# Kernel optimization log

Measured on AMD Instinct MI355X. Metric: run time of the kernel, lower is better.

Reference implementation:

```python
import jax, jax.numpy as jnp
import numpy as np

HEADS = 16
DIM_HEAD = 64
EPS = 1e-5


def _layernorm(x, w, b):
    mu = jnp.mean(x, axis=-1, keepdims=True)
    var = jnp.var(x, axis=-1, keepdims=True)
    return (x - mu) * jax.lax.rsqrt(var + EPS) * w + b


def setup_inputs() -> dict:
    key = jax.random.key(0)
    ks = jax.random.split(key, 6)
    B, F, Q, D = 8, 4096, 64, 1024
    inner = HEADS * DIM_HEAD  # 1024
    s = 0.02
    return {
        "features": jax.random.normal(ks[0], (B, F, D), jnp.float32),
        "latents": jax.random.normal(ks[1], (B, Q, D), jnp.float32),
        "lnm_w": jnp.ones((D,), jnp.float32),
        "lnm_b": jnp.zeros((D,), jnp.float32),
        "lnl_w": jnp.ones((D,), jnp.float32),
        "lnl_b": jnp.zeros((D,), jnp.float32),
        "Wq": jax.random.normal(ks[2], (D, inner), jnp.float32) * s,
        "Wk": jax.random.normal(ks[3], (D, inner), jnp.float32) * s,
        "Wv": jax.random.normal(ks[4], (D, inner), jnp.float32) * s,
        "Wo": jax.random.normal(ks[5], (inner, D), jnp.float32) * s,
    }


def reference(features, latents, lnm_w, lnm_b, lnl_w, lnl_b, Wq, Wk, Wv, Wo):
    B, Q = latents.shape[0], latents.shape[1]
    scale = DIM_HEAD ** (-0.5)

    x = _layernorm(features, lnm_w, lnm_b)           # (B, F, D)
    lat = _layernorm(latents, lnl_w, lnl_b)          # (B, Q, D)

    q = (lat @ Wq).reshape(B, Q, HEADS, DIM_HEAD).transpose(0, 2, 1, 3)  # b h q d
    kv_in = jnp.concatenate([x, lat], axis=1)        # (B, F+Q, D)
    FL = kv_in.shape[1]
    k = (kv_in @ Wk).reshape(B, FL, HEADS, DIM_HEAD).transpose(0, 2, 1, 3)  # b h f d
    v = (kv_in @ Wv).reshape(B, FL, HEADS, DIM_HEAD).transpose(0, 2, 1, 3)  # b h f d

    sim = jnp.einsum('bhqd,bhfd->bhqf', q * scale, k)
    alphas = jax.nn.softmax(sim, axis=-1)            # amax-subtract is folded into stable softmax
    out = jnp.einsum('bhqf,bhfv->bhqv', alphas, v)
    out = out.transpose(0, 2, 1, 3).reshape(B, Q, HEADS * DIM_HEAD)
    return out @ Wo
```

## Files before the change

### kernel.cpp

```cpp
#include <hip/hip_runtime.h>


typedef float   f32x4  __attribute__((ext_vector_type(4)));
typedef short   bf16x8 __attribute__((ext_vector_type(8)));

#define MFMA_BF16 __builtin_amdgcn_mfma_f32_16x16x32_bf16

__device__ __forceinline__ unsigned short f2bf(float f) {
  unsigned u = __float_as_uint(f);
  unsigned r = (u + 0x7fffu + ((u >> 16) & 1u)) >> 16;
  return (unsigned short)r;
}

__device__ __forceinline__ void gload_lds16(const unsigned short* g, unsigned short* l) {
  __builtin_amdgcn_global_load_lds(
      (const __attribute__((address_space(1))) unsigned int*)g,
      (__attribute__((address_space(3))) unsigned int*)l, 16, 0, 0);
}

__global__ __launch_bounds__(256) void ln_kernel(
    const float* __restrict__ features, const float* __restrict__ latents,
    const float* __restrict__ lnm_w, const float* __restrict__ lnm_b,
    const float* __restrict__ lnl_w, const float* __restrict__ lnl_b,
    unsigned short* __restrict__ kv_ln, unsigned short* __restrict__ lat_ln)
{
  const int row = blockIdx.x;
  const int b  = row / 4160;
  const int fi = row - b * 4160;
  const bool is_lat = fi >= 4096;
  const float* x = is_lat ? (latents + (size_t)(b * 64 + fi - 4096) * 1024)
                          : (features + (size_t)(b * 4096 + fi) * 1024);
  const float* wp = is_lat ? lnl_w : lnm_w;
  const float* bp = is_lat ? lnl_b : lnm_b;
  const int tid = threadIdx.x;

  float4 v = *(const float4*)(x + tid * 4);
  float s  = v.x + v.y + v.z + v.w;
  float s2 = v.x * v.x + v.y * v.y + v.z * v.z + v.w * v.w;
#pragma unroll
  for (int sh = 1; sh < 64; sh <<= 1) {
    s  += __shfl_xor(s,  sh, 64);
    s2 += __shfl_xor(s2, sh, 64);
  }
  __shared__ float red[8];
  if ((tid & 63) == 0) { red[tid >> 6] = s; red[4 + (tid >> 6)] = s2; }
  __syncthreads();
  s  = red[0] + red[1] + red[2] + red[3];
  s2 = red[4] + red[5] + red[6] + red[7];
  const float mu   = s * (1.0f / 1024.0f);
  const float var  = s2 * (1.0f / 1024.0f) - mu * mu;
  const float rstd = rsqrtf(var + 1e-5f);

  float4 w4 = *(const float4*)(wp + tid * 4);
  float4 b4 = *(const float4*)(bp + tid * 4);
  ushort4 o;
  o.x = f2bf((v.x - mu) * rstd * w4.x + b4.x);
  o.y = f2bf((v.y - mu) * rstd * w4.y + b4.y);
  o.z = f2bf((v.z - mu) * rstd * w4.z + b4.z);
  o.w = f2bf((v.w - mu) * rstd * w4.w + b4.w);
  *(ushort4*)(kv_ln + (size_t)row * 1024 + tid * 4) = o;
  if (is_lat)
    *(ushort4*)(lat_ln + (size_t)(b * 64 + fi - 4096) * 1024 + tid * 4) = o;
}

__global__ __launch_bounds__(256) void wcast_kernel(
    const float* __restrict__ Wq, const float* __restrict__ Wk,
    const float* __restrict__ Wv, const float* __restrict__ Wo,
    unsigned short* __restrict__ Wkv_t, unsigned short* __restrict__ Wq_t,
    unsigned short* __restrict__ Wo_t)
{
  __shared__ float tile[32][33];
  const int kt = blockIdx.x * 32, nt = blockIdx.y * 32;
  const int tx = threadIdx.x & 31, ty = threadIdx.x >> 5;

  const float* src; int nc; float scale = 1.0f;
  if (nt < 1024)      { src = Wk; nc = nt; }
  else if (nt < 2048) { src = Wv; nc = nt - 1024; }
  else if (nt < 3072) { src = Wq; nc = nt - 2048; scale = 0.125f; }
  else                { src = Wo; nc = nt - 3072; }

#pragma unroll
  for (int kk = 0; kk < 4; ++kk)
    tile[ty + kk * 8][tx] = src[(size_t)(kt + ty + kk * 8) * 1024 + nc + tx] * scale;
  __syncthreads();

#pragma unroll
  for (int nn = 0; nn < 4; ++nn) {
    const int ng = nt + ty + nn * 8;
    unsigned short* d;
    if (ng < 2048)      d = Wkv_t + (size_t)ng * 1024;
    else if (ng < 3072) d = Wq_t + (size_t)(ng - 2048) * 1024;
    else                d = Wo_t + (size_t)(ng - 3072) * 1024;
    d[kt + tx] = f2bf(tile[tx][ty + nn * 8]);
  }
}

__global__ __launch_bounds__(1024, 4) void gemm256_bf16(
    const unsigned short* __restrict__ A,
    const unsigned short* __restrict__ Bt,
    unsigned short* __restrict__ Kp, unsigned short* __restrict__ Vp,
    int M, int N, int K)
{
  __shared__ __align__(16) unsigned short lds[65536];
  const int tid  = threadIdx.x;
  const int wave = tid >> 6, lane = tid & 63;
  const int lo = lane & 15, hi = lane >> 4;
  const int wr = wave >> 2, wc = wave & 3;

  const int nbn = gridDim.x;
  int flat = blockIdx.y * nbn + blockIdx.x;
  const int nwg = nbn * gridDim.y;
  flat = (flat & 7) * (nwg >> 3) + (flat >> 3);
  const int bm = flat / nbn, bn = flat - bm * nbn;

  int srow, scol;
  {
    int off = tid * 16;
    int p = off ^ (((off >> 9) & 1) << 5);
    srow = ((p >> 10) << 4) + ((p & 1023) >> 6);
    scol = (p & 63) >> 1;
  }
  const unsigned short* pA = A  + (size_t)(bm * 256 + srow) * K + scol;
  const unsigned short* pB = Bt + (size_t)(bn * 256 + srow) * K + scol;

  f32x4 acc[4][4];
#pragma unroll
  for (int i = 0; i < 4; ++i)
#pragma unroll
    for (int j = 0; j < 4; ++j) acc[i][j] = (f32x4){0.f, 0.f, 0.f, 0.f};

  const int NT = K >> 5;

  gload_lds16(pA,      lds + 0 * 16384 + wave * 512);
  gload_lds16(pB,      lds + 0 * 16384 + 8192 + wave * 512);
  gload_lds16(pA + 32, lds + 1 * 16384 + wave * 512);
  gload_lds16(pB + 32, lds + 1 * 16384 + 8192 + wave * 512);
  asm volatile("s_waitcnt vmcnt(2)" ::: "memory");
  asm volatile("s_barrier" ::: "memory");

  const int swz = (lo * 32 + hi * 8) ^ ((lo & 8) << 1);

#define GPHASE(T, BUF, SBUF)                                                   \
  do {                                                                         \
    const bool st = (T) + 2 < NT;                                              \
    const unsigned short* bp = lds + (BUF) * 16384;                            \
    bf16x8 b0 = *(const bf16x8*)(bp + 8192 + (wc * 4 + 0) * 512 + swz);        \
    bf16x8 b1 = *(const bf16x8*)(bp + 8192 + (wc * 4 + 1) * 512 + swz);        \
    bf16x8 b2 = *(const bf16x8*)(bp + 8192 + (wc * 4 + 2) * 512 + swz);        \
    bf16x8 b3 = *(const bf16x8*)(bp + 8192 + (wc * 4 + 3) * 512 + swz);        \
    bf16x8 a0 = *(const bf16x8*)(bp + (wr * 4 + 0) * 512 + swz);               \
    bf16x8 a1 = *(const bf16x8*)(bp + (wr * 4 + 1) * 512 + swz);               \
    bf16x8 a2 = *(const bf16x8*)(bp + (wr * 4 + 2) * 512 + swz);               \
    bf16x8 a3 = *(const bf16x8*)(bp + (wr * 4 + 3) * 512 + swz);               \
    if (st) gload_lds16(pA + ((T) + 2) * 32, lds + (SBUF) * 16384 + wave * 512); \
    __builtin_amdgcn_s_setprio(1);                                             \
    acc[0][0] = MFMA_BF16(a0, b0, acc[0][0], 0, 0, 0);                         \
    acc[0][1] = MFMA_BF16(a0, b1, acc[0][1], 0, 0, 0);                         \
    acc[0][2] = MFMA_BF16(a0, b2, acc[0][2], 0, 0, 0);                         \
    acc[0][3] = MFMA_BF16(a0, b3, acc[0][3], 0, 0, 0);                         \
    acc[1][0] = MFMA_BF16(a1, b0, acc[1][0], 0, 0, 0);                         \
    acc[1][1] = MFMA_BF16(a1, b1, acc[1][1], 0, 0, 0);                         \
    acc[1][2] = MFMA_BF16(a1, b2, acc[1][2], 0, 0, 0);                         \
    acc[1][3] = MFMA_BF16(a1, b3, acc[1][3], 0, 0, 0);                         \
    __builtin_amdgcn_s_setprio(0);                                             \
    if (st) gload_lds16(pB + ((T) + 2) * 32, lds + (SBUF) * 16384 + 8192 + wave * 512); \
    __builtin_amdgcn_s_setprio(1);                                             \
    acc[2][0] = MFMA_BF16(a2, b0, acc[2][0], 0, 0, 0);                         \
    acc[2][1] = MFMA_BF16(a2, b1, acc[2][1], 0, 0, 0);                         \
    acc[2][2] = MFMA_BF16(a2, b2, acc[2][2], 0, 0, 0);                         \
    acc[2][3] = MFMA_BF16(a2, b3, acc[2][3], 0, 0, 0);                         \
    acc[3][0] = MFMA_BF16(a3, b0, acc[3][0], 0, 0, 0);                         \
    acc[3][1] = MFMA_BF16(a3, b1, acc[3][1], 0, 0, 0);                         \
    acc[3][2] = MFMA_BF16(a3, b2, acc[3][2], 0, 0, 0);                         \
    acc[3][3] = MFMA_BF16(a3, b3, acc[3][3], 0, 0, 0);                         \
    __builtin_amdgcn_s_setprio(0);                                             \
    if (st)                 { asm volatile("s_waitcnt vmcnt(2)" ::: "memory"); } \
    else if ((T) + 1 < NT)  { asm volatile("s_waitcnt vmcnt(0)" ::: "memory"); } \
    asm volatile("s_barrier" ::: "memory");                                    \
  } while (0)

  for (int t = 0; t < NT; t += 4) {
    GPHASE(t + 0, 0, 2);
    GPHASE(t + 1, 1, 3);
    GPHASE(t + 2, 2, 0);
    GPHASE(t + 3, 3, 1);
  }
#undef GPHASE

#pragma unroll
  for (int m = 0; m < 4; ++m) {
    const int grow0 = bm * 256 + wr * 64 + m * 16 + hi * 4;
#pragma unroll
    for (int n = 0; n < 4; ++n) {
      const int cfull = bn * 256 + wc * 64 + n * 16 + lo;
      unsigned short* plane = (cfull & 1024) ? Vp : Kp;
      const size_t pbase = (size_t)((cfull >> 6) & 15) * 2129920 + (cfull & 63);
#pragma unroll
      for (int r = 0; r < 4; ++r)
        plane[pbase + (size_t)(grow0 + r) * 64] = f2bf(acc[m][n][r]);
    }
  }
}

template <typename CT>
__global__ __launch_bounds__(256) void gemm_tn(
    const unsigned short* __restrict__ A,
    const unsigned short* __restrict__ Bt,
    CT* __restrict__ C, int M, int N, int K)
{
  __shared__ __align__(16) unsigned short sA[2][128 * 32];
  __shared__ __align__(16) unsigned short sB[2][128 * 32];
  const int tid  = threadIdx.x;
  const int wave = tid >> 6, lane = tid & 63;
  const int bm = blockIdx.y, bn = blockIdx.x;
  const int wr = wave >> 1, wc = wave & 1;
  const int lo = lane & 15, hi = lane >> 4;
  const int srow = lane >> 2, squad = lane & 3;

  const unsigned short* gA = A  + (size_t)(bm * 128 + srow) * K + squad * 8;
  const unsigned short* gB = Bt + (size_t)(bn * 128 + srow) * K + squad * 8;

  f32x4 acc[4][4];
#pragma unroll
  for (int i = 0; i < 4; ++i)
#pragma unroll
    for (int j = 0; j < 4; ++j) acc[i][j] = (f32x4){0.f, 0.f, 0.f, 0.f};

  const int kt = K >> 5;
#pragma unroll
  for (int c = 0; c < 2; ++c) {
    const int chunk = wave * 2 + c;
    gload_lds16(gA + (size_t)chunk * 16 * K, &sA[0][chunk * 512]);
    gload_lds16(gB + (size_t)chunk * 16 * K, &sB[0][chunk * 512]);
  }
  __syncthreads();

  int buf = 0;
  for (int t = 0; t < kt; ++t) {
    if (t + 1 < kt) {
      const int k0 = (t + 1) << 5;
#pragma unroll
      for (int c = 0; c < 2; ++c) {
        const int chunk = wave * 2 + c;
        gload_lds16(gA + (size_t)chunk * 16 * K + k0, &sA[buf ^ 1][chunk * 512]);
        gload_lds16(gB + (size_t)chunk * 16 * K + k0, &sB[buf ^ 1][chunk * 512]);
      }
    }
    bf16x8 af[4], bfr[4];
#pragma unroll
    for (int i = 0; i < 4; ++i) {
      af[i]  = *(const bf16x8*)&sA[buf][(wr * 64 + i * 16 + lo) * 32 + hi * 8];
      bfr[i] = *(const bf16x8*)&sB[buf][(wc * 64 + i * 16 + lo) * 32 + hi * 8];
    }
#pragma unroll
    for (int i = 0; i < 4; ++i)
#pragma unroll
      for (int j = 0; j < 4; ++j)
        acc[i][j] = MFMA_BF16(af[i], bfr[j], acc[i][j], 0, 0, 0);
    __syncthreads();
    buf ^= 1;
  }

#pragma unroll
  for (int i = 0; i < 4; ++i) {
    const int row0 = bm * 128 + wr * 64 + i * 16 + hi * 4;
#pragma unroll
    for (int j = 0; j < 4; ++j) {
      const int col = bn * 128 + wc * 64 + j * 16 + lo;
#pragma unroll
      for (int r = 0; r < 4; ++r) {
        const size_t idx = (size_t)(row0 + r) * N + col;
        if constexpr (sizeof(CT) == 2) C[idx] = (CT)f2bf(acc[i][j][r]);
        else                            C[idx] = acc[i][j][r];
      }
    }
  }
}

__global__ __launch_bounds__(256) void attn_kernel(
    const unsigned short* __restrict__ qws,
    const unsigned short* __restrict__ Kp, const unsigned short* __restrict__ Vp,
    float* __restrict__ pacc, float* __restrict__ pml)
{
  const int bhs = blockIdx.x;
  const int s = bhs & 7, h = (bhs >> 3) & 15, b = bhs >> 7;
  const int t0 = (s * 65) >> 3;
  const int t1 = ((s + 1) * 65) >> 3;
  const int tid = threadIdx.x;
  const int wave = tid >> 6, lane = tid & 63;
  const int lo = lane & 15, hi = lane >> 4;

  __shared__ __align__(16) unsigned short sK [64][72];
  __shared__ __align__(16) unsigned short sVT[64][72];
  __shared__ __align__(16) unsigned short sP [4][16][72];

  bf16x8 qf[2];
  {
    const unsigned short* p = qws + (size_t)(b * 64 + wave * 16 + lo) * 1024 + h * 64 + hi * 8;
    qf[0] = *(const bf16x8*)p;
    qf[1] = *(const bf16x8*)(p + 32);
  }
  float m[4] = {-1e30f, -1e30f, -1e30f, -1e30f};
  float l[4] = {0.f, 0.f, 0.f, 0.f};
  f32x4 acc[4];
#pragma unroll
  for (int i = 0; i < 4; ++i) acc[i] = (f32x4){0.f, 0.f, 0.f, 0.f};

  const int frow = tid >> 2, c4 = tid & 3;
  const size_t hbase = (size_t)h * 2129920;

  bf16x8 kreg[2], vreg[2];
  {
    const size_t rb = hbase + (size_t)(b * 4160 + t0 * 64 + frow) * 64;
#pragma unroll
    for (int rr = 0; rr < 2; ++rr) {
      const int d0 = rr * 32 + c4 * 8;
      kreg[rr] = *(const bf16x8*)(Kp + rb + d0);
      vreg[rr] = *(const bf16x8*)(Vp + rb + d0);
    }
  }

  for (int t = t0; t < t1; ++t) {
    __syncthreads();
#pragma unroll
    for (int rr = 0; rr < 2; ++rr) {
      const int d0 = rr * 32 + c4 * 8;
      *(bf16x8*)&sK[frow][d0] = kreg[rr];
#pragma unroll
      for (int j = 0; j < 8; ++j) sVT[d0 + j][frow] = (unsigned short)vreg[rr][j];
    }
    __syncthreads();
    if (t + 1 < t1) {
      const size_t rb = hbase + (size_t)(b * 4160 + (t + 1) * 64 + frow) * 64;
#pragma unroll
      for (int rr = 0; rr < 2; ++rr) {
        const int d0 = rr * 32 + c4 * 8;
        kreg[rr] = *(const bf16x8*)(Kp + rb + d0);
        vreg[rr] = *(const bf16x8*)(Vp + rb + d0);
      }
    }

    f32x4 sim[4];
#pragma unroll
    for (int nf = 0; nf < 4; ++nf) {
      f32x4 a0 = (f32x4){0.f, 0.f, 0.f, 0.f};
#pragma unroll
      for (int ks = 0; ks < 2; ++ks) {
        bf16x8 kf = *(const bf16x8*)&sK[nf * 16 + lo][ks * 32 + hi * 8];
        a0 = MFMA_BF16(qf[ks], kf, a0, 0, 0, 0);
      }
      sim[nf] = a0;
    }

    float pr[4][4];
    float corr[4];
#pragma unroll
    for (int r = 0; r < 4; ++r) {
      float tm = fmaxf(fmaxf(sim[0][r], sim[1][r]), fmaxf(sim[2][r], sim[3][r]));
#pragma unroll
      for (int sh = 1; sh < 16; sh <<= 1) tm = fmaxf(tm, __shfl_xor(tm, sh, 64));
      const float mn = fmaxf(m[r], tm);
      corr[r] = __expf(m[r] - mn);
      float rs = 0.f;
#pragma unroll
      for (int nf = 0; nf < 4; ++nf) {
        float p = __expf(sim[nf][r] - mn);
        pr[r][nf] = p;
        rs += p;
      }
#pragma unroll
      for (int sh = 1; sh < 16; sh <<= 1) rs += __shfl_xor(rs, sh, 64);
      l[r] = l[r] * corr[r] + rs;
      m[r] = mn;
    }

    {
      const int r2 = lane & 3;
      float csel = r2 == 0 ? corr[0] : r2 == 1 ? corr[1] : r2 == 2 ? corr[2] : corr[3];
      const int src = ((lane & 15) >> 2) * 16 + (lane & 3);
      const float cacc = __shfl(csel, src, 64);
#pragma unroll
      for (int i = 0; i < 4; ++i) acc[i] *= cacc;
    }

#pragma unroll
    for (int r = 0; r < 4; ++r)
#pragma unroll
      for (int nf = 0; nf < 4; ++nf)
        sP[wave][hi * 4 + r][nf * 16 + lo] = f2bf(pr[r][nf]);

#pragma unroll
    for (int ks = 0; ks < 2; ++ks) {
      bf16x8 pf = *(const bf16x8*)&sP[wave][lo][ks * 32 + hi * 8];
#pragma unroll
      for (int i = 0; i < 4; ++i) {
        bf16x8 vf = *(const bf16x8*)&sVT[i * 16 + lo][ks * 32 + hi * 8];
        acc[i] = MFMA_BF16(vf, pf, acc[i], 0, 0, 0);
      }
    }
  }

  if (lo == 0) {
#pragma unroll
    for (int r = 0; r < 4; ++r) {
      pml[bhs * 128 + wave * 16 + hi * 4 + r]      = m[r];
      pml[bhs * 128 + 64 + wave * 16 + hi * 4 + r] = l[r];
    }
  }
#pragma unroll
  for (int i = 0; i < 4; ++i)
#pragma unroll
    for (int r = 0; r < 4; ++r)
      pacc[bhs * 4096 + (i * 16 + hi * 4 + r) * 64 + wave * 16 + lo] = acc[i][r];
}

__global__ __launch_bounds__(256) void attn_combine(
    const float* __restrict__ pacc, const float* __restrict__ pml,
    unsigned short* __restrict__ attn_out)
{
  const int bh = blockIdx.x;
  const int b = bh >> 4, h = bh & 15;
  const int t = threadIdx.x;
  const int q = t & 63, dg = t >> 6;
  const int base = bh << 3;

  float mm[8], ll[8];
#pragma unroll
  for (int s = 0; s < 8; ++s) {
    mm[s] = pml[(base + s) * 128 + q];
    ll[s] = pml[(base + s) * 128 + 64 + q];
  }
  float M = mm[0];
#pragma unroll
  for (int s = 1; s < 8; ++s) M = fmaxf(M, mm[s]);
  float e[8];
  float L = 0.f;
#pragma unroll
  for (int s = 0; s < 8; ++s) { e[s] = __expf(mm[s] - M); L += e[s] * ll[s]; }
  const float inv = 1.0f / L;

#pragma unroll
  for (int dd = 0; dd < 16; ++dd) {
    const int d = dg * 16 + dd;
    float v = 0.f;
#pragma unroll
    for (int s = 0; s < 8; ++s)
      v += e[s] * pacc[(base + s) * 4096 + d * 64 + q];
    attn_out[(size_t)(b * 64 + q) * 1024 + h * 64 + d] = f2bf(v * inv);
  }
}

extern "C" void kernel_launch(void* const* d_in, const int* in_sizes, int n_in,
                              void* d_out, int out_size, void* d_ws, size_t ws_size,
                              hipStream_t stream) {
  const float* features = (const float*)d_in[0];
  const float* latents  = (const float*)d_in[1];
  const float* lnm_w = (const float*)d_in[2];
  const float* lnm_b = (const float*)d_in[3];
  const float* lnl_w = (const float*)d_in[4];
  const float* lnl_b = (const float*)d_in[5];
  const float* Wq = (const float*)d_in[6];
  const float* Wk = (const float*)d_in[7];
  const float* Wv = (const float*)d_in[8];
  const float* Wo = (const float*)d_in[9];
  float* out = (float*)d_out;

  char* ws = (char*)d_ws;
  unsigned short* kv_ln    = (unsigned short*)(ws);
  unsigned short* Wkv_t    = (unsigned short*)(ws + 68157440);
  unsigned short* Wq_t     = (unsigned short*)(ws + 72351744);
  unsigned short* Wo_t     = (unsigned short*)(ws + 74448896);
  unsigned short* lat_ln   = (unsigned short*)(ws + 76546048);
  unsigned short* q_ws     = (unsigned short*)(ws + 77594624);
  unsigned short* attn_out = (unsigned short*)(ws + 78643200);
  unsigned short* Kp       = (unsigned short*)(ws + 79691776);
  unsigned short* Vp       = (unsigned short*)(ws + 147849216);
  float* pacc = (float*)(ws);
  float* pml  = (float*)(ws + 16777216);

  ln_kernel<<<33280, 256, 0, stream>>>(features, latents, lnm_w, lnm_b, lnl_w, lnl_b,
                                       kv_ln, lat_ln);
  wcast_kernel<<<dim3(32, 128), 256, 0, stream>>>(Wq, Wk, Wv, Wo, Wkv_t, Wq_t, Wo_t);
  gemm256_bf16<<<dim3(8, 130), 1024, 0, stream>>>(kv_ln, Wkv_t, Kp, Vp, 33280, 2048, 1024);
  gemm_tn<unsigned short><<<dim3(8, 4), 256, 0, stream>>>(lat_ln, Wq_t, q_ws, 512, 1024, 1024);
  attn_kernel<<<1024, 256, 0, stream>>>(q_ws, Kp, Vp, pacc, pml);
  attn_combine<<<128, 256, 0, stream>>>(pacc, pml, attn_out);
  gemm_tn<float><<<dim3(8, 4), 256, 0, stream>>>(attn_out, Wo_t, out, 512, 1024, 1024);
}
```

Measured before the change: 296.6 us.

## Shrink KV projection GEMM tile to 256x128 with 512 threads and triple-buffered LDS

```diff
diff --git a/kernel.cpp b/kernel.cpp
--- a/kernel.cpp
+++ b/kernel.cpp
@@ -95,17 +95,17 @@
   }
 }
 
-__global__ __launch_bounds__(1024, 4) void gemm256_bf16(
+__global__ __launch_bounds__(512, 4) void gemm256_bf16(
     const unsigned short* __restrict__ A,
     const unsigned short* __restrict__ Bt,
     unsigned short* __restrict__ Kp, unsigned short* __restrict__ Vp,
     int M, int N, int K)
 {
-  __shared__ __align__(16) unsigned short lds[65536];
+  __shared__ __align__(16) unsigned short lds[36864];
   const int tid  = threadIdx.x;
   const int wave = tid >> 6, lane = tid & 63;
   const int lo = lane & 15, hi = lane >> 4;
-  const int wr = wave >> 2, wc = wave & 3;
+  const int wr = wave >> 1, wc = wave & 1;
 
   const int nbn = gridDim.x;
   int flat = blockIdx.y * nbn + blockIdx.x;
@@ -113,15 +113,26 @@
   flat = (flat & 7) * (nwg >> 3) + (flat >> 3);
   const int bm = flat / nbn, bn = flat - bm * nbn;
 
-  int srow, scol;
+  int garA[2], gakA[2];
+#pragma unroll
+  for (int gi = 0; gi < 2; ++gi) {
+    int off = gi * 8192 + tid * 16;
+    int p = off ^ (((off >> 9) & 1) << 5);
+    int s = p >> 10, q = p & 1023;
+    garA[gi] = (s >> 1) * 16 + (q >> 6) + 128 * (s & 1);
+    gakA[gi] = (q & 63) >> 1;
+  }
+  int grB, gkB;
   {
     int off = tid * 16;
     int p = off ^ (((off >> 9) & 1) << 5);
-    srow = ((p >> 10) << 4) + ((p & 1023) >> 6);
-    scol = (p & 63) >> 1;
-  }
-  const unsigned short* pA = A  + (size_t)(bm * 256 + srow) * K + scol;
-  const unsigned short* pB = Bt + (size_t)(bn * 256 + srow) * K + scol;
+    int s = p >> 10, q = p & 1023;
+    grB = (s >> 1) * 16 + (q >> 6) + 64 * (s & 1);
+    gkB = (q & 63) >> 1;
+  }
+  const unsigned short* pA0 = A  + (size_t)(bm * 256 + garA[0]) * K + gakA[0];
+  const unsigned short* pA1 = A  + (size_t)(bm * 256 + garA[1]) * K + gakA[1];
+  const unsigned short* pB  = Bt + (size_t)(bn * 128 + grB)     * K + gkB;
 
   f32x4 acc[4][4];
 #pragma unroll
@@ -131,70 +142,65 @@
 
   const int NT = K >> 5;
 
-  gload_lds16(pA,      lds + 0 * 16384 + wave * 512);
-  gload_lds16(pB,      lds + 0 * 16384 + 8192 + wave * 512);
-  gload_lds16(pA + 32, lds + 1 * 16384 + wave * 512);
-  gload_lds16(pB + 32, lds + 1 * 16384 + 8192 + wave * 512);
-  asm volatile("s_waitcnt vmcnt(2)" ::: "memory");
+#pragma unroll
+  for (int tt = 0; tt < 2; ++tt) {
+    unsigned short* bb = lds + tt * 12288;
+    gload_lds16(pA0 + tt * 32, bb + wave * 512);
+    gload_lds16(pA1 + tt * 32, bb + 4096 + wave * 512);
+    gload_lds16(pB  + tt * 32, bb + 8192 + wave * 512);
+  }
+  asm volatile("s_waitcnt vmcnt(3)" ::: "memory");
   asm volatile("s_barrier" ::: "memory");
 
   const int swz = (lo * 32 + hi * 8) ^ ((lo & 8) << 1);
-
-#define GPHASE(T, BUF, SBUF)                                                   \
-  do {                                                                         \
-    const bool st = (T) + 2 < NT;                                              \
-    const unsigned short* bp = lds + (BUF) * 16384;                            \
-    bf16x8 b0 = *(const bf16x8*)(bp + 8192 + (wc * 4 + 0) * 512 + swz);        \
-    bf16x8 b1 = *(const bf16x8*)(bp + 8192 + (wc * 4 + 1) * 512 + swz);        \
-    bf16x8 b2 = *(const bf16x8*)(bp + 8192 + (wc * 4 + 2) * 512 + swz);        \
-    bf16x8 b3 = *(const bf16x8*)(bp + 8192 + (wc * 4 + 3) * 512 + swz);        \
-    bf16x8 a0 = *(const bf16x8*)(bp + (wr * 4 + 0) * 512 + swz);               \
-    bf16x8 a1 = *(const bf16x8*)(bp + (wr * 4 + 1) * 512 + swz);               \
-    bf16x8 a2 = *(const bf16x8*)(bp + (wr * 4 + 2) * 512 + swz);               \
-    bf16x8 a3 = *(const bf16x8*)(bp + (wr * 4 + 3) * 512 + swz);               \
-    if (st) gload_lds16(pA + ((T) + 2) * 32, lds + (SBUF) * 16384 + wave * 512); \
-    __builtin_amdgcn_s_setprio(1);                                             \
-    acc[0][0] = MFMA_BF16(a0, b0, acc[0][0], 0, 0, 0);                         \
-    acc[0][1] = MFMA_BF16(a0, b1, acc[0][1], 0, 0, 0);                         \
-    acc[0][2] = MFMA_BF16(a0, b2, acc[0][2], 0, 0, 0);                         \
-    acc[0][3] = MFMA_BF16(a0, b3, acc[0][3], 0, 0, 0);                         \
-    acc[1][0] = MFMA_BF16(a1, b0, acc[1][0], 0, 0, 0);                         \
-    acc[1][1] = MFMA_BF16(a1, b1, acc[1][1], 0, 0, 0);                         \
-    acc[1][2] = MFMA_BF16(a1, b2, acc[1][2], 0, 0, 0);                         \
-    acc[1][3] = MFMA_BF16(a1, b3, acc[1][3], 0, 0, 0);                         \
-    __builtin_amdgcn_s_setprio(0);                                             \
-    if (st) gload_lds16(pB + ((T) + 2) * 32, lds + (SBUF) * 16384 + 8192 + wave * 512); \
-    __builtin_amdgcn_s_setprio(1);                                             \
-    acc[2][0] = MFMA_BF16(a2, b0, acc[2][0], 0, 0, 0);                         \
-    acc[2][1] = MFMA_BF16(a2, b1, acc[2][1], 0, 0, 0);                         \
-    acc[2][2] = MFMA_BF16(a2, b2, acc[2][2], 0, 0, 0);                         \
-    acc[2][3] = MFMA_BF16(a2, b3, acc[2][3], 0, 0, 0);                         \
-    acc[3][0] = MFMA_BF16(a3, b0, acc[3][0], 0, 0, 0);                         \
-    acc[3][1] = MFMA_BF16(a3, b1, acc[3][1], 0, 0, 0);                         \
-    acc[3][2] = MFMA_BF16(a3, b2, acc[3][2], 0, 0, 0);                         \
-    acc[3][3] = MFMA_BF16(a3, b3, acc[3][3], 0, 0, 0);                         \
-    __builtin_amdgcn_s_setprio(0);                                             \
-    if (st)                 { asm volatile("s_waitcnt vmcnt(2)" ::: "memory"); } \
-    else if ((T) + 1 < NT)  { asm volatile("s_waitcnt vmcnt(0)" ::: "memory"); } \
-    asm volatile("s_barrier" ::: "memory");                                    \
-  } while (0)
-
-  for (int t = 0; t < NT; t += 4) {
-    GPHASE(t + 0, 0, 2);
-    GPHASE(t + 1, 1, 3);
-    GPHASE(t + 2, 2, 0);
-    GPHASE(t + 3, 3, 1);
-  }
-#undef GPHASE
+  int aAddr[4], bAddr[4];
+#pragma unroll
+  for (int m = 0; m < 4; ++m)
+    aAddr[m] = ((((wr & 1) * 4 + m) * 2) + (wr >> 1)) * 512 + swz;
+#pragma unroll
+  for (int n = 0; n < 4; ++n)
+    bAddr[n] = 8192 + (n * 2 + wc) * 512 + swz;
+
+  int cur = 0;
+  for (int t = 0; t < NT; ++t) {
+    const unsigned short* bp = lds + cur * 12288;
+    bf16x8 af[4], bf[4];
+#pragma unroll
+    for (int m = 0; m < 4; ++m) af[m] = *(const bf16x8*)(bp + aAddr[m]);
+#pragma unroll
+    for (int n = 0; n < 4; ++n) bf[n] = *(const bf16x8*)(bp + bAddr[n]);
+
+    if (t + 2 < NT) {
+      int s2 = cur + 2; if (s2 >= 3) s2 -= 3;
+      unsigned short* db = lds + s2 * 12288;
+      const int koff = (t + 2) * 32;
+      gload_lds16(pA0 + koff, db + wave * 512);
+      gload_lds16(pA1 + koff, db + 4096 + wave * 512);
+      gload_lds16(pB  + koff, db + 8192 + wave * 512);
+    }
+
+    __builtin_amdgcn_s_setprio(1);
+#pragma unroll
+    for (int m = 0; m < 4; ++m)
+#pragma unroll
+      for (int n = 0; n < 4; ++n)
+        acc[m][n] = MFMA_BF16(af[m], bf[n], acc[m][n], 0, 0, 0);
+    __builtin_amdgcn_s_setprio(0);
+
+    if (t + 2 < NT)      { asm volatile("s_waitcnt vmcnt(3)" ::: "memory"); }
+    else if (t + 1 < NT) { asm volatile("s_waitcnt vmcnt(0)" ::: "memory"); }
+    asm volatile("s_barrier" ::: "memory");
+    cur = (cur == 2) ? 0 : cur + 1;
+  }
 
 #pragma unroll
   for (int m = 0; m < 4; ++m) {
     const int grow0 = bm * 256 + wr * 64 + m * 16 + hi * 4;
 #pragma unroll
     for (int n = 0; n < 4; ++n) {
-      const int cfull = bn * 256 + wc * 64 + n * 16 + lo;
-      unsigned short* plane = (cfull & 1024) ? Vp : Kp;
-      const size_t pbase = (size_t)((cfull >> 6) & 15) * 2129920 + (cfull & 63);
+      const int gcol = bn * 128 + wc * 64 + n * 16 + lo;
+      unsigned short* plane = (gcol & 1024) ? Vp : Kp;
+      const size_t pbase = (size_t)((gcol >> 6) & 15) * 2129920 + (gcol & 63);
 #pragma unroll
       for (int r = 0; r < 4; ++r)
         plane[pbase + (size_t)(grow0 + r) * 64] = f2bf(acc[m][n][r]);
@@ -481,7 +487,7 @@
   ln_kernel<<<33280, 256, 0, stream>>>(features, latents, lnm_w, lnm_b, lnl_w, lnl_b,
                                        kv_ln, lat_ln);
   wcast_kernel<<<dim3(32, 128), 256, 0, stream>>>(Wq, Wk, Wv, Wo, Wkv_t, Wq_t, Wo_t);
-  gemm256_bf16<<<dim3(8, 130), 1024, 0, stream>>>(kv_ln, Wkv_t, Kp, Vp, 33280, 2048, 1024);
+  gemm256_bf16<<<dim3(16, 130), 512, 0, stream>>>(kv_ln, Wkv_t, Kp, Vp, 33280, 2048, 1024);
   gemm_tn<unsigned short><<<dim3(8, 4), 256, 0, stream>>>(lat_ln, Wq_t, q_ws, 512, 1024, 1024);
   attn_kernel<<<1024, 256, 0, stream>>>(q_ws, Kp, Vp, pacc, pml);
   attn_combine<<<128, 256, 0, stream>>>(pacc, pml, attn_out);
```

Result: faster. 289.3 us (-2.5%).
